# Kernel optimization log

Hardware: AMD Instinct MI355X
Metric: run time of the kernel (lower is better)

Reference implementation:

```python
import jax, jax.numpy as jnp
import numpy as np


def setup_inputs() -> dict:
    key = jax.random.key(0)
    ks = jax.random.split(key, 20)
    B, T, N, Cin = 1, 12, 30000, 16
    H, Hc = 64, 128
    O, KW = 12, 128
    E2 = 480000  # half of edges; symmetrized below -> E = 960000
    s = 0.05
    node_features = jax.random.normal(ks[0], (B, T, N, Cin), jnp.float32)
    src = jax.random.randint(ks[1], (T, E2), 0, N)
    dst = jax.random.randint(ks[2], (T, E2), 0, N)
    edge_index = jnp.concatenate(
        [jnp.stack([src, dst], axis=1), jnp.stack([dst, src], axis=1)], axis=-1)  # [T,2,E]
    return dict(
        node_features=node_features,
        edge_index=edge_index,
        gru_Wih0=jax.random.normal(ks[3], (2, 3 * H, Cin), jnp.float32) * s,
        gru_Whh0=jax.random.normal(ks[4], (2, 3 * H, H), jnp.float32) * s,
        gru_bih0=jax.random.normal(ks[5], (2, 3 * H), jnp.float32) * s,
        gru_bhh0=jax.random.normal(ks[6], (2, 3 * H), jnp.float32) * s,
        gru_Wih1=jax.random.normal(ks[7], (2, 3 * H, 2 * H), jnp.float32) * s,
        gru_Whh1=jax.random.normal(ks[8], (2, 3 * H, H), jnp.float32) * s,
        gru_bih1=jax.random.normal(ks[9], (2, 3 * H), jnp.float32) * s,
        gru_bhh1=jax.random.normal(ks[10], (2, 3 * H), jnp.float32) * s,
        ln_scale=jnp.ones((H,), jnp.float32),
        ln_bias=jnp.zeros((H,), jnp.float32),
        cheb_W=jax.random.normal(ks[11], (3, H, Hc), jnp.float32) * s,
        cheb_b=jnp.zeros((Hc,), jnp.float32),
        conv_W=jax.random.normal(ks[12], (O, T, 1, KW), jnp.float32) * s,
        conv_b=jnp.zeros((O,), jnp.float32),
    )


def reference(node_features, edge_index, gru_Wih0, gru_Whh0, gru_bih0, gru_bhh0,
              gru_Wih1, gru_Whh1, gru_bih1, gru_bhh1, ln_scale, ln_bias,
              cheb_W, cheb_b, conv_W, conv_b):
    B, T, N, Cin = node_features.shape
    H = gru_Whh0.shape[-1]
    M = B * N
    x = node_features.transpose(0, 2, 1, 3).reshape(M, T, Cin)

    def bigru(x, Wih, Whh, bih, bhh):
        # PyTorch bidirectional GRU layer (eval mode -> no dropout)
        outs = []
        for d, rev in ((0, False), (1, True)):
            gi = jnp.einsum('mtd,gd->tmg', x, Wih[d]) + bih[d]  # [T, M, 3H]
            def step(h, g, d=d):
                gh = h @ Whh[d].T + bhh[d]
                ir, iz, inn = jnp.split(g, 3, axis=-1)
                hr, hz, hn = jnp.split(gh, 3, axis=-1)
                r = jax.nn.sigmoid(ir + hr)
                z = jax.nn.sigmoid(iz + hz)
                n = jnp.tanh(inn + r * hn)
                h = (1.0 - z) * n + z * h
                return h, h
            h0 = jnp.zeros((x.shape[0], Whh.shape[-1]), x.dtype)
            _, ys = jax.lax.scan(step, h0, gi, reverse=rev)
            outs.append(jnp.swapaxes(ys, 0, 1))
        return jnp.concatenate(outs, axis=-1)  # [M, T, 2H]

    x = bigru(x, gru_Wih0, gru_Whh0, gru_bih0, gru_bhh0)
    x = bigru(x, gru_Wih1, gru_Whh1, gru_bih1, gru_bhh1)
    # reshape(M,T,2,H), LayerNorm(H), take direction 1 == slice then LayerNorm
    xb = x[:, :, H:]
    mu = jnp.mean(xb, axis=-1, keepdims=True)
    var = jnp.mean((xb - mu) ** 2, axis=-1, keepdims=True)
    xb = (xb - mu) * jax.lax.rsqrt(var + 1e-5) * ln_scale + ln_bias
    xs_t = jnp.moveaxis(xb.reshape(B, N, T, H), 2, 0).reshape(T, M, H)  # per-timestep [M,H]

    E = edge_index.shape[-1]
    N_ITER = 75  # power-iteration steps for lambda_max (scipy eigs equivalent)

    def cheb_step(_, inp):
        x_t, edges = inp  # x_t [M,H], edges [2,E]
        row, col = edges[0], edges[1]
        deg = jax.ops.segment_sum(jnp.ones((E,), x_t.dtype), row, num_segments=M)
        def Lmv(v):  # unnormalized Laplacian (D - A) matvec
            return deg * v - jax.ops.segment_sum(v[col], row, num_segments=M)
        v0 = jnp.full((M,), 1.0 / np.sqrt(M), x_t.dtype)
        def pit(i, v):
            w = Lmv(v)
            return w / (jnp.linalg.norm(w) + 1e-12)
        v = jax.lax.fori_loop(0, N_ITER, pit, v0)
        lam = jnp.vdot(v, Lmv(v))  # lambda_max of D - A (LaplacianLambdaMax default)
        # ChebConv sym-normalized, rescaled Laplacian: L_hat = (2/lam)*(I - D^-1/2 A D^-1/2) - I
        dinv = jnp.where(deg > 0, 1.0 / jnp.sqrt(jnp.maximum(deg, 1.0)), 0.0)
        we = (-2.0 / lam) * dinv[row] * dinv[col]  # off-diagonal weights
        diag = 2.0 / lam - 1.0                      # diagonal (all nodes)
        def Lhat(xm):
            return diag * xm + jax.ops.segment_sum(we[:, None] * xm[col], row, num_segments=M)
        Tx0 = x_t
        Tx1 = Lhat(Tx0)
        Tx2 = 2.0 * Lhat(Tx1) - Tx0
        out = Tx0 @ cheb_W[0] + Tx1 @ cheb_W[1] + Tx2 @ cheb_W[2] + cheb_b
        return 0, out

    _, emb = jax.lax.scan(cheb_step, 0, (xs_t, edge_index))  # [T, M, Hc]
    Hc = cheb_W.shape[-1]
    emb = jnp.moveaxis(emb.reshape(T, B, N, Hc), 0, 1)  # [B, T, N, Hc]
    # Conv2d(T -> O, kernel (1,KW)) followed by [:,:,:,-1]: only last window matters
    KW = conv_W.shape[-1]
    out = jnp.einsum('btnk,otk->bno', emb[..., Hc - KW:], conv_W[:, :, 0, :]) + conv_b
    return jax.nn.sigmoid(out)  # [B, N, num_for_predict]
```

## Files before the change

### kernel.cpp

```cpp
#include <hip/hip_runtime.h>
#include <hip/hip_bf16.h>

#define DEV __device__ __forceinline__

constexpr int Mn  = 30000;
constexpr int Tt  = 12;
constexpr int CIN = 16;
constexpr int Hh  = 64;
constexpr int Gg  = 192;
constexpr int C2  = 128;
constexpr int Ee  = 960000;
constexpr int HC  = 128;
constexpr int Oo  = 12;
constexpr int KW  = 128;
constexpr int SEGS= 938;
constexpr int NB  = 235;
constexpr int EPB = 8192;
constexpr int BPT = 118;
constexpr int CHK = 21;
constexpr int RC  = 1440;
constexpr int NRND= 76;
constexpr int NF4A= 21*256;
constexpr int NF4B= 20*104 + 44;

DEV float bf2f(__hip_bfloat16 v){ return __bfloat162float(v); }
DEV __hip_bfloat16 f2bf(float v){ return __float2bfloat16(v); }
DEV float sigm(float x){ return __builtin_amdgcn_rcpf(1.f + __expf(-x)); }
DEV float tanh_f(float x){ return 1.f - 2.f*__builtin_amdgcn_rcpf(__expf(2.f*x) + 1.f); }

DEV float aload_f(const float* p){ return __hip_atomic_load(p, __ATOMIC_RELAXED, __HIP_MEMORY_SCOPE_AGENT); }
DEV void  astore_f(float* p, float v){ __hip_atomic_store(p, v, __ATOMIC_RELAXED, __HIP_MEMORY_SCOPE_AGENT); }
DEV int   aload_i(const int* p){ return __hip_atomic_load(p, __ATOMIC_RELAXED, __HIP_MEMORY_SCOPE_AGENT); }
DEV void  astore_i(int* p, int v){ __hip_atomic_store(p, v, __ATOMIC_RELAXED, __HIP_MEMORY_SCOPE_AGENT); }
DEV unsigned long long aload_u64(const unsigned long long* p){ return __hip_atomic_load(p, __ATOMIC_RELAXED, __HIP_MEMORY_SCOPE_AGENT); }
DEV void astore_u64(unsigned long long* p, unsigned long long v){ __hip_atomic_store(p, v, __ATOMIC_RELAXED, __HIP_MEMORY_SCOPE_AGENT); }

typedef short bfrag8 __attribute__((ext_vector_type(8)));
typedef float ffrag4 __attribute__((ext_vector_type(4)));

DEV int off_h(int row, int col){
  return row*64 + ((((col >> 3) ^ (row & 7)) << 3) | (col & 7));
}

DEV short bfbits(float v){ __hip_bfloat16 b = f2bf(v); return *reinterpret_cast<short*>(&b); }

__global__ void k_init(int* bcnt, int* bfill, int* flagA, unsigned long long* pbB){
  int i = blockIdx.x*256 + threadIdx.x;
  if (i < Tt*CHK*16){ flagA[i] = 0; pbB[i] = 0ull; }
  if (i < Tt*NB){ bcnt[i] = 0; bfill[i] = 0; }
}

__global__ __launch_bounds__(256) void k_bcnt(const int* __restrict__ ei, int* __restrict__ bcnt){
  __shared__ int h[NB];
  const int b = blockIdx.x;
  const int w = (b & 7)*177 + (b >> 3);
  const int t = w / BPT, ch = w - t*BPT;
  const int e0 = ch*EPB;
  const int tid = threadIdx.x;
  for (int i = tid; i < NB; i += 256) h[i] = 0;
  __syncthreads();
  #pragma unroll
  for (int i = 0; i < 32; ++i){
    int e = e0 + i*256 + tid;
    if (e < Ee){
      int r = ei[(size_t)(t*2)*Ee + e];
      atomicAdd(&h[r >> 7], 1);
    }
  }
  __syncthreads();
  for (int i = tid; i < NB; i += 256){
    int c = h[i];
    if (c > 0) atomicAdd(&bcnt[t*NB + i], c);
  }
}

__global__ __launch_bounds__(256) void k_bscan(const int* __restrict__ bcnt, int* __restrict__ rpb){
  int t = blockIdx.x, tid = threadIdx.x;
  __shared__ int ps[256];
  int v = (tid < NB) ? bcnt[t*NB + tid] : 0;
  ps[tid] = v;
  __syncthreads();
  for (int o = 1; o < 256; o <<= 1){
    int x = (tid >= o) ? ps[tid-o] : 0;
    __syncthreads();
    ps[tid] += x;
    __syncthreads();
  }
  if (tid < NB) rpb[t*(NB+1) + tid] = ps[tid] - v;
  if (tid == 255) rpb[t*(NB+1) + NB] = ps[NB-1];
}

__global__ __launch_bounds__(256) void k_part2(const int* __restrict__ ei, const int* __restrict__ rpb,
    int* __restrict__ bfill, unsigned* __restrict__ pair){
  __shared__ int hcnt[NB];
  __shared__ int hbase[NB];
  const int b = blockIdx.x;
  const int w = (b & 7)*177 + (b >> 3);
  const int t = w / BPT, ch = w - t*BPT;
  const int e0 = ch*EPB;
  const int tid = threadIdx.x;
  for (int i = tid; i < NB; i += 256) hcnt[i] = 0;
  __syncthreads();
  unsigned key[32];
  #pragma unroll
  for (int i = 0; i < 32; ++i){
    int e = e0 + i*256 + tid;
    unsigned k = 0xFFFFFFFFu;
    if (e < Ee){
      int r = ei[(size_t)(t*2)*Ee + e];
      int c = ei[(size_t)(t*2+1)*Ee + e];
      k = ((unsigned)r << 16) | (unsigned)c;
      atomicAdd(&hcnt[r >> 7], 1);
    }
    key[i] = k;
  }
  __syncthreads();
  for (int i = tid; i < NB; i += 256){
    int cnt = hcnt[i];
    int base = (cnt > 0) ? atomicAdd(&bfill[t*NB + i], cnt) : 0;
    hbase[i] = rpb[t*(NB+1) + i] + base;
  }
  __syncthreads();
  for (int i = tid; i < NB; i += 256) hcnt[i] = 0;
  __syncthreads();
  #pragma unroll
  for (int i = 0; i < 32; ++i){
    unsigned k = key[i];
    if (k != 0xFFFFFFFFu){
      int r = (int)(k >> 16);
      int bk = r >> 7;
      int pos = atomicAdd(&hcnt[bk], 1);
      pair[(size_t)t*Ee + hbase[bk] + pos] = ((unsigned)(r & 127) << 16) | (k & 0xFFFFu);
    }
  }
}

__global__ __launch_bounds__(256) void k_csr2(const int* __restrict__ rpb, const unsigned* __restrict__ pair,
    unsigned short* __restrict__ col16, int* __restrict__ rp, int* __restrict__ deg){
  __shared__ unsigned short cols_s[9216];
  __shared__ int lcnt[128], lfill[128];
  __shared__ int ps[256];
  const int blk = blockIdx.x;
  const int t = blk / NB, bk = blk - t*NB;
  const int r0 = bk << 7;
  const int nr = (r0 + 128 <= Mn) ? 128 : (Mn - r0);
  const int base = rpb[t*(NB+1) + bk];
  const int cnt  = rpb[t*(NB+1) + bk + 1] - base;
  const int tid = threadIdx.x;
  if (tid < 128) lcnt[tid] = 0;
  __syncthreads();
  for (int i = tid; i < cnt; i += 256){
    unsigned v = pair[(size_t)t*Ee + base + i];
    atomicAdd(&lcnt[v >> 16], 1);
  }
  __syncthreads();
  int v2 = (tid < 128) ? lcnt[tid] : 0;
  ps[tid] = v2;
  __syncthreads();
  for (int o = 1; o < 128; o <<= 1){
    int x = (tid >= o) ? ps[tid-o] : 0;
    __syncthreads();
    ps[tid] += x;
    __syncthreads();
  }
  if (tid < 128){
    int excl = ps[tid] - v2;
    lfill[tid] = excl;
    if (tid < nr){
      rp[t*(Mn+1) + r0 + tid] = base + excl;
      deg[t*Mn + r0 + tid] = v2;
    }
  }
  if (bk == NB-1 && tid == 0) rp[t*(Mn+1) + Mn] = base + cnt;
  __syncthreads();
  for (int i = tid; i < cnt; i += 256){
    unsigned v = pair[(size_t)t*Ee + base + i];
    int pos = atomicAdd(&lfill[v >> 16], 1);
    cols_s[pos] = (unsigned short)(v & 0xFFFFu);
  }
  __syncthreads();
  for (int i = tid; i < cnt; i += 256)
    col16[(size_t)t*Ee + base + i] = cols_s[i];
}

__global__ void k_dinv(const int* __restrict__ deg, float* __restrict__ dinv){
  int i = blockIdx.x*256 + threadIdx.x;
  if (i < Tt*Mn){ int d = deg[i]; dinv[i] = (d > 0) ? rsqrtf((float)d) : 0.f; }
}

__global__ __launch_bounds__(256) void k_gru0(
    const float* __restrict__ nf, const float* __restrict__ Wih, const float* __restrict__ Whh,
    const float* __restrict__ bih, const float* __restrict__ bhh, __hip_bfloat16* __restrict__ y0)
{
  __shared__ __hip_bfloat16 xp[Tt*32*32];
  __shared__ __hip_bfloat16 h_hi[32*64];
  __shared__ __hip_bfloat16 h_lo[32*64];
  const int tid = threadIdx.x;
  const int m0  = blockIdx.x*32;
  const int lane = tid & 63, wv = tid >> 6;
  const int lr = lane & 15, lq = lane >> 4;
  for (int idx = tid; idx < Tt*32*CIN; idx += 256){
    int t = idx >> 9; int row = (idx >> 4) & 31; int k = idx & 15;
    int m = m0 + row;
    float v = (m < Mn) ? nf[((size_t)t*Mn + m)*CIN + k] : 0.f;
    __hip_bfloat16 hi = f2bf(v);
    xp[(t*32 + row)*32 + k]      = hi;
    xp[(t*32 + row)*32 + 16 + k] = f2bf(v - bf2f(hi));
  }
  for (int d = 0; d < 2; ++d){
    bfrag8 Bh[3][2], Bx[3];
    float b_r, b_z, b_in, b_hn;
    {
      const float* Wh = Whh + (size_t)d*Gg*Hh;
      const float* Wx = Wih + (size_t)d*Gg*CIN;
      #pragma unroll
      for (int c = 0; c < 3; ++c){
        int g = (wv + 4*c)*16 + lr;
        #pragma unroll
        for (int ks = 0; ks < 2; ++ks){
          bfrag8 f;
          #pragma unroll
          for (int r = 0; r < 8; ++r) f[r] = bfbits(Wh[(size_t)g*Hh + ks*32 + lq*8 + r]);
          Bh[c][ks] = f;
        }
        bfrag8 fx;
        #pragma unroll
        for (int r = 0; r < 8; ++r) fx[r] = bfbits(Wx[(size_t)g*CIN + ((lq*8 + r) & 15)]);
        Bx[c] = fx;
      }
      int j = wv*16 + lr;
      b_r  = bih[d*Gg + j]        + bhh[d*Gg + j];
      b_z  = bih[d*Gg + Hh + j]   + bhh[d*Gg + Hh + j];
      b_in = bih[d*Gg + 2*Hh + j];
      b_hn = bhh[d*Gg + 2*Hh + j];
    }
    float hreg[8];
    #pragma unroll
    for (int q = 0; q < 8; ++q) hreg[q] = 0.f;
    for (int i = tid; i < 32*64; i += 256){ h_hi[i] = f2bf(0.f); h_lo[i] = f2bf(0.f); }
    __syncthreads();
    for (int step = 0; step < Tt; ++step){
      int t = d ? (Tt-1-step) : step;
      bfrag8 xa[2], hhf[2][2], hlf[2][2];
      #pragma unroll
      for (int rt = 0; rt < 2; ++rt){
        int row = rt*16 + lr;
        xa[rt] = *(const bfrag8*)&xp[(t*32 + row)*32 + lq*8];
        #pragma unroll
        for (int ks = 0; ks < 2; ++ks){
          int e = off_h(row, ks*32 + lq*8);
          hhf[rt][ks] = *(const bfrag8*)&h_hi[e];
          hlf[rt][ks] = *(const bfrag8*)&h_lo[e];
        }
      }
      ffrag4 Cr[2], Cz[2], Cai[2], Cah[2];
      #pragma unroll
      for (int rt = 0; rt < 2; ++rt){
        ffrag4 z4 = (ffrag4){0.f,0.f,0.f,0.f};
        Cr[rt]  = __builtin_amdgcn_mfma_f32_16x16x32_bf16(xa[rt], Bx[0], z4, 0,0,0);
        Cz[rt]  = __builtin_amdgcn_mfma_f32_16x16x32_bf16(xa[rt], Bx[1], z4, 0,0,0);
        Cai[rt] = __builtin_amdgcn_mfma_f32_16x16x32_bf16(xa[rt], Bx[2], z4, 0,0,0);
        Cah[rt] = z4;
        #pragma unroll
        for (int ks = 0; ks < 2; ++ks){
          Cr[rt]  = __builtin_amdgcn_mfma_f32_16x16x32_bf16(hhf[rt][ks], Bh[0][ks], Cr[rt], 0,0,0);
          Cr[rt]  = __builtin_amdgcn_mfma_f32_16x16x32_bf16(hlf[rt][ks], Bh[0][ks], Cr[rt], 0,0,0);
          Cz[rt]  = __builtin_amdgcn_mfma_f32_16x16x32_bf16(hhf[rt][ks], Bh[1][ks], Cz[rt], 0,0,0);
          Cz[rt]  = __builtin_amdgcn_mfma_f32_16x16x32_bf16(hlf[rt][ks], Bh[1][ks], Cz[rt], 0,0,0);
          Cah[rt] = __builtin_amdgcn_mfma_f32_16x16x32_bf16(hhf[rt][ks], Bh[2][ks], Cah[rt], 0,0,0);
          Cah[rt] = __builtin_amdgcn_mfma_f32_16x16x32_bf16(hlf[rt][ks], Bh[2][ks], Cah[rt], 0,0,0);
        }
      }
      __syncthreads();
      #pragma unroll
      for (int rt = 0; rt < 2; ++rt){
        #pragma unroll
        for (int q = 0; q < 4; ++q){
          float r = sigm(Cr[rt][q] + b_r);
          float z = sigm(Cz[rt][q] + b_z);
          float n = tanh_f((Cai[rt][q] + b_in) + r*(Cah[rt][q] + b_hn));
          float h = (1.f - z)*n + z*hreg[rt*4+q];
          hreg[rt*4+q] = h;
          __hip_bfloat16 hi = f2bf(h);
          int e = off_h(rt*16 + lq*4 + q, wv*16 + lr);
          h_hi[e] = hi;
          h_lo[e] = f2bf(h - bf2f(hi));
        }
      }
      __syncthreads();
      {
        int row = tid >> 3, cg = tid & 7;
        int m = m0 + row;
        if (m < Mn){
          float4 v = *(const float4*)&h_hi[off_h(row, cg*8)];
          *(float4*)&y0[((size_t)t*Mn + m)*C2 + d*Hh + cg*8] = v;
        }
      }
    }
    __syncthreads();
  }
}

__global__ void k_wcvt(const float* __restrict__ W, __hip_bfloat16* __restrict__ Wbf){
  int i = blockIdx.x*256 + threadIdx.x;
  if (i < Gg*C2) Wbf[i] = f2bf(W[i]);
}

__global__ __launch_bounds__(256) void k_gi1m(const __hip_bfloat16* __restrict__ y0,
    const __hip_bfloat16* __restrict__ Wbf, const float* __restrict__ bih, __hip_bfloat16* __restrict__ gi)
{
  const int wid  = (blockIdx.x*256 + threadIdx.x) >> 6;
  const int lane = threadIdx.x & 63;
  if (wid >= Tt*SEGS) return;
  const int t = wid / SEGS, seg = wid - t*SEGS;
  const int m0 = seg*32;
  const int lr = lane & 15, lq = lane >> 4;
  const __hip_bfloat16* yb = y0 + (size_t)t*Mn*C2;

  ffrag4 acc[2][12];
  #pragma unroll
  for (int i = 0; i < 2; ++i){
    #pragma unroll
    for (int n = 0; n < 12; ++n) acc[i][n] = (ffrag4){0.f,0.f,0.f,0.f};
  }
  #pragma unroll
  for (int ks = 0; ks < 4; ++ks){
    const int ko = ks*32 + lq*8;
    bfrag8 a0 = *(const bfrag8*)(yb + (size_t)(m0 + lr     )*C2 + ko);
    bfrag8 a1 = *(const bfrag8*)(yb + (size_t)(m0 + 16 + lr)*C2 + ko);
    #pragma unroll
    for (int nt = 0; nt < 12; ++nt){
      bfrag8 b = *(const bfrag8*)(Wbf + (size_t)(nt*16 + lr)*C2 + ko);
      acc[0][nt] = __builtin_amdgcn_mfma_f32_16x16x32_bf16(a0, b, acc[0][nt], 0, 0, 0);
      acc[1][nt] = __builtin_amdgcn_mfma_f32_16x16x32_bf16(a1, b, acc[1][nt], 0, 0, 0);
    }
  }
  ushort4* go = (ushort4*)gi;
  #pragma unroll
  for (int i = 0; i < 2; ++i){
    #pragma unroll
    for (int nt = 0; nt < 12; ++nt){
      float bb = bih[nt*16 + lr];
      ushort4 pk;
      pk.x = (unsigned short)bfbits(acc[i][nt][0] + bb);
      pk.y = (unsigned short)bfbits(acc[i][nt][1] + bb);
      pk.z = (unsigned short)bfbits(acc[i][nt][2] + bb);
      pk.w = (unsigned short)bfbits(acc[i][nt][3] + bb);
      go[((((size_t)t*SEGS + seg)*2 + i)*12 + nt)*64 + lane] = pk;
    }
  }
}

__global__ __launch_bounds__(256) void k_gru1r(const __hip_bfloat16* __restrict__ gi,
    const float* __restrict__ Whh, const float* __restrict__ bhh,
    const float* __restrict__ lns, const float* __restrict__ lnb,
    __hip_bfloat16* __restrict__ xbt)
{
  __shared__ __hip_bfloat16 h_hi[32*64];
  __shared__ __hip_bfloat16 h_lo[32*64];
  __shared__ float h_f32[32*72];
  __shared__ float sc[Hh], bs[Hh];
  const int tid = threadIdx.x;
  const int seg = blockIdx.x;
  const int m0  = seg*32;
  const int lane = tid & 63, wv = tid >> 6;
  const int lr = lane & 15, lq = lane >> 4;
  bfrag8 Bh[3][2];
  float b_r, b_z, b_hn;
  #pragma unroll
  for (int c = 0; c < 3; ++c){
    int g = (wv + 4*c)*16 + lr;
    #pragma unroll
    for (int ks = 0; ks < 2; ++ks){
      bfrag8 f;
      #pragma unroll
      for (int r = 0; r < 8; ++r) f[r] = bfbits(Whh[(size_t)g*Hh + ks*32 + lq*8 + r]);
      Bh[c][ks] = f;
    }
  }
  {
    int j = wv*16 + lr;
    b_r  = bhh[j];
    b_z  = bhh[Hh + j];
    b_hn = bhh[2*Hh + j];
  }
  if (tid < Hh){ sc[tid] = lns[tid]; bs[tid] = lnb[tid]; }
  float hreg[8];
  #pragma unroll
  for (int q = 0; q < 8; ++q) hreg[q] = 0.f;
  for (int i = tid; i < 32*64; i += 256){ h_hi[i] = f2bf(0.f); h_lo[i] = f2bf(0.f); }
  __syncthreads();
  const ushort4* gbase = (const ushort4*)gi;
  for (int step = 0; step < Tt; ++step){
    int t = Tt-1-step;
    ffrag4 Cr[2], Cz[2], Cai[2], Cah[2];
    #pragma unroll
    for (int rt = 0; rt < 2; ++rt){
      size_t base = (((size_t)t*SEGS + seg)*2 + rt)*12;
      ushort4 gr4 = gbase[(base + wv     )*64 + lane];
      ushort4 gz4 = gbase[(base + wv + 4 )*64 + lane];
      ushort4 gn4 = gbase[(base + wv + 8 )*64 + lane];
      __hip_bfloat16 b;
      ffrag4 cr, cz, cn;
      b = *(__hip_bfloat16*)&gr4.x; cr[0] = bf2f(b);
      b = *(__hip_bfloat16*)&gr4.y; cr[1] = bf2f(b);
      b = *(__hip_bfloat16*)&gr4.z; cr[2] = bf2f(b);
      b = *(__hip_bfloat16*)&gr4.w; cr[3] = bf2f(b);
      b = *(__hip_bfloat16*)&gz4.x; cz[0] = bf2f(b);
      b = *(__hip_bfloat16*)&gz4.y; cz[1] = bf2f(b);
      b = *(__hip_bfloat16*)&gz4.z; cz[2] = bf2f(b);
      b = *(__hip_bfloat16*)&gz4.w; cz[3] = bf2f(b);
      b = *(__hip_bfloat16*)&gn4.x; cn[0] = bf2f(b);
      b = *(__hip_bfloat16*)&gn4.y; cn[1] = bf2f(b);
      b = *(__hip_bfloat16*)&gn4.z; cn[2] = bf2f(b);
      b = *(__hip_bfloat16*)&gn4.w; cn[3] = bf2f(b);
      Cr[rt] = cr; Cz[rt] = cz; Cai[rt] = cn;
      Cah[rt] = (ffrag4){0.f,0.f,0.f,0.f};
    }
    bfrag8 hhf[2][2], hlf[2][2];
    #pragma unroll
    for (int rt = 0; rt < 2; ++rt){
      int row = rt*16 + lr;
      #pragma unroll
      for (int ks = 0; ks < 2; ++ks){
        int e = off_h(row, ks*32 + lq*8);
        hhf[rt][ks] = *(const bfrag8*)&h_hi[e];
        hlf[rt][ks] = *(const bfrag8*)&h_lo[e];
      }
    }
    #pragma unroll
    for (int rt = 0; rt < 2; ++rt){
      #pragma unroll
      for (int ks = 0; ks < 2; ++ks){
        Cr[rt]  = __builtin_amdgcn_mfma_f32_16x16x32_bf16(hhf[rt][ks], Bh[0][ks], Cr[rt], 0,0,0);
        Cr[rt]  = __builtin_amdgcn_mfma_f32_16x16x32_bf16(hlf[rt][ks], Bh[0][ks], Cr[rt], 0,0,0);
        Cz[rt]  = __builtin_amdgcn_mfma_f32_16x16x32_bf16(hhf[rt][ks], Bh[1][ks], Cz[rt], 0,0,0);
        Cz[rt]  = __builtin_amdgcn_mfma_f32_16x16x32_bf16(hlf[rt][ks], Bh[1][ks], Cz[rt], 0,0,0);
        Cah[rt] = __builtin_amdgcn_mfma_f32_16x16x32_bf16(hhf[rt][ks], Bh[2][ks], Cah[rt], 0,0,0);
        Cah[rt] = __builtin_amdgcn_mfma_f32_16x16x32_bf16(hlf[rt][ks], Bh[2][ks], Cah[rt], 0,0,0);
      }
    }
    __syncthreads();
    #pragma unroll
    for (int rt = 0; rt < 2; ++rt){
      #pragma unroll
      for (int q = 0; q < 4; ++q){
        float r = sigm(Cr[rt][q] + b_r);
        float z = sigm(Cz[rt][q] + b_z);
        float n = tanh_f(Cai[rt][q] + r*(Cah[rt][q] + b_hn));
        float h = (1.f - z)*n + z*hreg[rt*4+q];
        hreg[rt*4+q] = h;
        __hip_bfloat16 hi = f2bf(h);
        int row = rt*16 + lq*4 + q;
        int e = off_h(row, wv*16 + lr);
        h_hi[e] = hi;
        h_lo[e] = f2bf(h - bf2f(hi));
        h_f32[row*72 + wv*16 + lr] = h;
      }
    }
    __syncthreads();
    {
      int row = tid >> 3, l = tid & 7;
      float4 v0 = *(const float4*)&h_f32[row*72 + l*8];
      float4 v1 = *(const float4*)&h_f32[row*72 + l*8 + 4];
      float vals[8] = {v0.x, v0.y, v0.z, v0.w, v1.x, v1.y, v1.z, v1.w};
      float s1 = 0.f, s2 = 0.f;
      #pragma unroll
      for (int q = 0; q < 8; ++q){ s1 += vals[q]; s2 += vals[q]*vals[q]; }
      #pragma unroll
      for (int off = 1; off <= 4; off <<= 1){ s1 += __shfl_xor(s1, off); s2 += __shfl_xor(s2, off); }
      float mu  = s1 * (1.f/64.f);
      float var = s2 * (1.f/64.f) - mu*mu;
      float rs  = rsqrtf(var + 1e-5f);
      int m = m0 + row;
      if (m < Mn){
        __hip_bfloat16 ob[8];
        #pragma unroll
        for (int q = 0; q < 8; ++q){ int j = l*8 + q; ob[q] = f2bf((vals[q]-mu)*rs*sc[j] + bs[j]); }
        *(float4*)&xbt[((size_t)t*Mn + m)*Hh + l*8] = *(float4*)ob;
      }
    }
    __syncthreads();
  }
}

__global__ __launch_bounds__(1024) void k_pitall(const int* __restrict__ rp,
    const unsigned short* __restrict__ col, float* __restrict__ urb,
    int* __restrict__ flagA, unsigned long long* __restrict__ pbB,
    float* __restrict__ lamc)
{
  __shared__ alignas(16) float u_s[Mn];
  __shared__ float redw[16];
  __shared__ float s_nrm;
  __shared__ int s_goA, s_goB;
  const int b = blockIdx.x;
  const int t = b / CHK, ch = b - t*CHK;
  const int r0 = ch*RC;
  const int r1 = (r0 + RC < Mn) ? r0 + RC : Mn;
  const int tid = threadIdx.x;
  const int lane = tid & 63;
  const int wv   = tid >> 6;
  const unsigned short* cp = col + (size_t)t*Ee;
  const int fS = t*CHK*16;
  const int pB = t*CHK*16;
  const int m0r = r0 + tid;
  const int m1r = m0r + 1024;
  int rb0 = 0, re0 = 0, rb1 = 0, re1 = 0;
  {
    const int* rpt = rp + t*(Mn+1);
    if (m0r < r1){ rb0 = rpt[m0r]; re0 = rpt[m0r+1]; }
    if (m1r < r1){ rb1 = rpt[m1r]; re1 = rpt[m1r+1]; }
  }
  if (tid == 0){ s_nrm = 1.0f; s_goA = 0; s_goB = 0; }
  __syncthreads();
  for (int r = 1; r <= NRND; ++r){
    const int fin = (r == NRND);
    if (r == 1){
      for (int i = tid; i < Mn; i += 1024) u_s[i] = 0.005773502691896258f;
    } else {
      const int rr = r - 1;
      const float4* u4 = (const float4*)(urb + (size_t)rr*(Tt*Mn) + (size_t)t*Mn);
      float4* s4 = (float4*)u_s;
      if (wv == 0){
        const bool mine = lane < CHK;
        for (;;){ int v = mine ? aload_i(&flagA[fS + lane*16]) : 0x7FFFFFFF;
                  if (__all(v >= rr)) break; __builtin_amdgcn_s_sleep(4); }
        if (lane == 0) __hip_atomic_store(&s_goA, rr, __ATOMIC_RELAXED, __HIP_MEMORY_SCOPE_WORKGROUP);
      } else {
        while (__hip_atomic_load(&s_goA, __ATOMIC_RELAXED, __HIP_MEMORY_SCOPE_WORKGROUP) < rr)
          __builtin_amdgcn_s_sleep(2);
      }
      asm volatile("" ::: "memory");
      for (int i = tid; i < NF4A; i += 1024){
        int idx = (i >> 8)*360 + (i & 255);
        s4[idx] = u4[idx];
      }
      unsigned long long pv = 0;
      if (wv == 0){
        const bool mine = lane < CHK;
        for (;;){ pv = mine ? aload_u64(&pbB[(size_t)(pB + lane*16) + (rr & 1)*8])
                            : ((unsigned long long)rr << 32);
                  if (__all((int)(pv >> 32) == rr)) break; __builtin_amdgcn_s_sleep(4); }
        if (lane == 0) __hip_atomic_store(&s_goB, rr, __ATOMIC_RELAXED, __HIP_MEMORY_SCOPE_WORKGROUP);
      } else {
        while (__hip_atomic_load(&s_goB, __ATOMIC_RELAXED, __HIP_MEMORY_SCOPE_WORKGROUP) < rr)
          __builtin_amdgcn_s_sleep(2);
      }
      asm volatile("" ::: "memory");
      for (int i = tid; i < NF4B; i += 1024){
        int ck = i/104, off = i - ck*104;
        int idx = ck*360 + 256 + off;
        s4[idx] = u4[idx];
      }
      if (wv == 0){
        float p = (lane < CHK) ? __uint_as_float((unsigned)pv) : 0.f;
        #pragma unroll
        for (int o2 = 1; o2 < 32; o2 <<= 1) p += __shfl_xor(p, o2);
        if (tid == 0) s_nrm = p;
      }
    }
    __syncthreads();
    const float inv_s = fin ? 1.f : 1.f/(sqrtf(s_nrm) + 1e-12f);
    float* u_ot = urb + (size_t)r*(Tt*Mn);
    float local = 0.f;
    if (m0r < r1){
      float s = 0.f;
      int i = rb0;
      for (; i < re0 && (i & 3); ++i) s += u_s[cp[i]];
      for (; i + 4 <= re0; i += 4){
        ushort4 c4 = *(const ushort4*)(cp + i);
        s += (u_s[c4.x] + u_s[c4.y]) + (u_s[c4.z] + u_s[c4.w]);
      }
      for (; i < re0; ++i) s += u_s[cp[i]];
      float uv = u_s[m0r];
      float wv2 = (float)(re0 - rb0)*uv - s;
      if (!fin){ float o = inv_s*wv2; astore_f(&u_ot[t*Mn + m0r], o); local += o*o; }
      else local += uv*wv2;
    }
    asm volatile("s_waitcnt vmcnt(0)" ::: "memory");
    __syncthreads();
    if (tid == 0) astore_i(&flagA[fS + ch*16], r);
    if (m1r < r1){
      float s = 0.f;
      int i = rb1;
      for (; i < re1 && (i & 3); ++i) s += u_s[cp[i]];
      for (; i + 4 <= re1; i += 4){
        ushort4 c4 = *(const ushort4*)(cp + i);
        s += (u_s[c4.x] + u_s[c4.y]) + (u_s[c4.z] + u_s[c4.w]);
      }
      for (; i < re1; ++i) s += u_s[cp[i]];
      float uv = u_s[m1r];
      float wv2 = (float)(re1 - rb1)*uv - s;
      if (!fin){ float o = inv_s*wv2; astore_f(&u_ot[t*Mn + m1r], o); local += o*o; }
      else local += uv*wv2;
    }
    #pragma unroll
    for (int o2 = 1; o2 < 64; o2 <<= 1) local += __shfl_xor(local, o2);
    if ((tid & 63) == 0) redw[tid >> 6] = local;
    asm volatile("s_waitcnt vmcnt(0)" ::: "memory");
    __syncthreads();
    if (tid < 64){
      float tot = (tid < 16) ? redw[tid] : 0.f;
      #pragma unroll
      for (int o2 = 1; o2 < 16; o2 <<= 1) tot += __shfl_xor(tot, o2);
      if (tid == 0){
        unsigned long long out = ((unsigned long long)r << 32)
                               | (unsigned long long)__float_as_uint(tot);
        astore_u64(&pbB[(size_t)(pB + ch*16) + (r & 1)*8], out);
      }
    }
  }
  if (ch == 0 && tid < 64){
    const bool mine = lane < CHK;
    unsigned long long pv = 0;
    for (;;){ pv = mine ? aload_u64(&pbB[(size_t)(pB + lane*16) + (NRND & 1)*8])
                        : ((unsigned long long)NRND << 32);
              if (__all((int)(pv >> 32) == NRND)) break; __builtin_amdgcn_s_sleep(4); }
    float p = mine ? __uint_as_float((unsigned)pv) : 0.f;
    #pragma unroll
    for (int o2 = 1; o2 < 32; o2 <<= 1) p += __shfl_xor(p, o2);
    if (tid == 0){
      float nn = sqrtf(s_nrm) + 1e-12f;
      float lam = p / (nn*nn);
      lamc[2*t+0] = -2.f/lam;
      lamc[2*t+1] =  2.f/lam - 1.f;
    }
  }
}

__global__ __launch_bounds__(256) void k_cheb(const __hip_bfloat16* __restrict__ xin,
    const __hip_bfloat16* __restrict__ xb0, __hip_bfloat16* __restrict__ outp,
    const int* __restrict__ rp, const unsigned short* __restrict__ col,
    const float* __restrict__ dinv, const float* __restrict__ lamc, float s1, float s2)
{
  const int blk = blockIdx.x;
  const int w = (blk & 7)*11250 + (blk >> 3);
  const int gw = w*4 + (threadIdx.x >> 6);
  const int lane = threadIdx.x & 63;
  int t = gw / Mn, m = gw - t*Mn;
  float coef = lamc[2*t], diag = lamc[2*t+1];
  const __hip_bfloat16* xt = xin + (size_t)t*Mn*Hh;
  const float* dv = dinv + t*Mn;
  float acc = diag * bf2f(xt[(size_t)m*Hh + lane]);
  float cdm = coef * dv[m];
  int bgn = rp[t*(Mn+1)+m], end = rp[t*(Mn+1)+m+1];
  const unsigned short* cp = col + (size_t)t*Ee;
  int i = bgn;
  for (; i < end && (i & 3); ++i){ int c = cp[i]; acc += (cdm*dv[c])*bf2f(xt[(size_t)c*Hh + lane]); }
  for (; i + 4 <= end; i += 4){
    ushort4 c4 = *(const ushort4*)(cp + i);
    float w0 = cdm*dv[c4.x], w1 = cdm*dv[c4.y], w2 = cdm*dv[c4.z], w3 = cdm*dv[c4.w];
    acc += w0*bf2f(xt[(size_t)c4.x*Hh + lane]);
    acc += w1*bf2f(xt[(size_t)c4.y*Hh + lane]);
    acc += w2*bf2f(xt[(size_t)c4.z*Hh + lane]);
    acc += w3*bf2f(xt[(size_t)c4.w*Hh + lane]);
  }
  for (; i < end; ++i){ int c = cp[i]; acc += (cdm*dv[c])*bf2f(xt[(size_t)c*Hh + lane]); }
  float o = s1*acc;
  if (s2 != 0.f) o += s2*bf2f(xb0[(size_t)gw*Hh + lane]);
  outp[(size_t)gw*Hh + lane] = f2bf(o);
}

__global__ void k_ww(const float* __restrict__ chebW, const float* __restrict__ chebb,
    const float* __restrict__ convW, const float* __restrict__ convb, float* __restrict__ WW, float* __restrict__ c0)
{
  int idx = blockIdx.x*256 + threadIdx.x;
  if (idx < 3*Tt*Hh*Oo){
    int oc = idx % Oo; int j = (idx/Oo) % Hh; int t = (idx/(Oo*Hh)) % Tt; int i = idx/(Oo*Hh*Tt);
    const float* cw = chebW + ((size_t)i*Hh + j)*HC + (HC-KW);
    const float* vw = convW + ((size_t)oc*Tt + t)*KW;
    float s = 0.f;
    for (int k = 0; k < KW; ++k) s += cw[k]*vw[k];
    WW[idx] = s;
  }
  if (blockIdx.x == 0 && threadIdx.x < Oo){
    int oc = threadIdx.x;
    float s = convb[oc];
    for (int t = 0; t < Tt; ++t){
      const float* vw = convW + ((size_t)oc*Tt + t)*KW;
      for (int k = 0; k < KW; ++k) s += chebb[(HC-KW)+k]*vw[k];
    }
    c0[oc] = s;
  }
}

__global__ __launch_bounds__(256) void k_final(const __hip_bfloat16* __restrict__ tx0,
    const __hip_bfloat16* __restrict__ tx1, const __hip_bfloat16* __restrict__ tx2,
    const float* __restrict__ WW, const float* __restrict__ c0, float* __restrict__ outp)
{
  __shared__ float xs[64][65];
  __shared__ float ww[64][12];
  const int tid = threadIdx.x;
  const int n0 = blockIdx.x*64;
  const int n = tid & 63, ob = (tid >> 6)*3;
  float acc[3] = {0.f, 0.f, 0.f};
  for (int it = 0; it < 3*Tt; ++it){
    int ii = it / Tt, t = it % Tt;
    const __hip_bfloat16* tx = (ii == 0) ? tx0 : (ii == 1) ? tx1 : tx2;
    __syncthreads();
    for (int idx = tid; idx < 64*64; idx += 256){
      int mm = idx >> 6, j = idx & 63;
      int m = n0 + mm;
      xs[mm][j] = (m < Mn) ? bf2f(tx[((size_t)t*Mn + m)*Hh + j]) : 0.f;
    }
    for (int idx = tid; idx < 64*Oo; idx += 256)
      ((float*)ww)[idx] = WW[((size_t)(ii*Tt + t)*Hh)*Oo + idx];
    __syncthreads();
    #pragma unroll 8
    for (int j = 0; j < 64; ++j){
      float x = xs[n][j];
      acc[0] += x*ww[j][ob+0];
      acc[1] += x*ww[j][ob+1];
      acc[2] += x*ww[j][ob+2];
    }
  }
  int m = n0 + n;
  if (m < Mn){
    #pragma unroll
    for (int q = 0; q < 3; ++q) outp[(size_t)m*Oo + ob + q] = sigm(acc[q] + c0[ob+q]);
  }
}

extern "C" void kernel_launch(void* const* d_in, const int* in_sizes, int n_in,
                              void* d_out, int out_size, void* d_ws, size_t ws_size,
                              hipStream_t stream)
{
  const float* nf    = (const float*)d_in[0];
  const int*   ei    = (const int*)d_in[1];
  const float* Wih0  = (const float*)d_in[2];
  const float* Whh0  = (const float*)d_in[3];
  const float* bih0  = (const float*)d_in[4];
  const float* bhh0  = (const float*)d_in[5];
  const float* Wih1  = (const float*)d_in[6];
  const float* Whh1  = (const float*)d_in[7];
  const float* bih1  = (const float*)d_in[8];
  const float* bhh1  = (const float*)d_in[9];
  const float* lns   = (const float*)d_in[10];
  const float* lnb   = (const float*)d_in[11];
  const float* chebW = (const float*)d_in[12];
  const float* chebb = (const float*)d_in[13];
  const float* convW = (const float*)d_in[14];
  const float* convb = (const float*)d_in[15];
  float* outp = (float*)d_out;

  char* base = (char*)d_ws;
  size_t off = 0;
  auto alloc = [&](size_t bytes)->char*{ char* p = base + off; off += (bytes + 255) & ~(size_t)255; return p; };

  __hip_bfloat16* y0  = (__hip_bfloat16*)alloc((size_t)Tt*Mn*C2*2);
  __hip_bfloat16* tx1 = y0;
  __hip_bfloat16* tx2 = y0 + (size_t)Tt*Mn*Hh;
  __hip_bfloat16* gi  = (__hip_bfloat16*)alloc((size_t)Tt*SEGS*32*Gg*2);
  unsigned* pair = (unsigned*)gi;
  float* urb = (float*)gi;
  __hip_bfloat16* xbt = (__hip_bfloat16*)alloc((size_t)Tt*Mn*Hh*2);
  unsigned short* col16 = (unsigned short*)alloc((size_t)Tt*Ee*2);
  int*   deg  = (int*)alloc((size_t)Tt*Mn*4);
  int*   rp   = (int*)alloc((size_t)Tt*(Mn+1)*4);
  int*   bcnt = (int*)alloc((size_t)Tt*NB*4);
  int*   bfill= (int*)alloc((size_t)Tt*NB*4);
  int*   rpb  = (int*)alloc((size_t)Tt*(NB+1)*4);
  float* dinv = (float*)alloc((size_t)Tt*Mn*4);
  float* lamc = (float*)alloc((size_t)2*Tt*4);
  float* WW   = (float*)alloc((size_t)3*Tt*Hh*Oo*4);
  float* c0   = (float*)alloc((size_t)Oo*4);
  __hip_bfloat16* Wbf = (__hip_bfloat16*)alloc((size_t)Gg*C2*2);
  int*   flagA = (int*)alloc((size_t)Tt*CHK*16*4);
  unsigned long long* pbB = (unsigned long long*)alloc((size_t)Tt*CHK*16*8);
  (void)ws_size; (void)in_sizes; (void)n_in; (void)out_size;

  k_init<<<16, 256, 0, stream>>>(bcnt, bfill, flagA, pbB);
  k_bcnt<<<Tt*BPT, 256, 0, stream>>>(ei, bcnt);
  k_bscan<<<Tt, 256, 0, stream>>>(bcnt, rpb);
  k_part2<<<Tt*BPT, 256, 0, stream>>>(ei, rpb, bfill, pair);
  k_csr2<<<Tt*NB, 256, 0, stream>>>(rpb, pair, col16, rp, deg);
  k_dinv<<<(Tt*Mn + 255)/256, 256, 0, stream>>>(deg, dinv);

  k_wcvt<<<(Gg*C2 + 255)/256, 256, 0, stream>>>(Wih1 + (size_t)Gg*C2, Wbf);
  k_gru0<<<SEGS, 256, 0, stream>>>(nf, Wih0, Whh0, bih0, bhh0, y0);
  {
    int waves = Tt*SEGS;
    k_gi1m<<<(waves + 3)/4, 256, 0, stream>>>(y0, Wbf, bih1 + Gg, gi);
  }
  k_gru1r<<<SEGS, 256, 0, stream>>>(gi, Whh1 + (size_t)Gg*Hh, bhh1 + Gg, lns, lnb, xbt);

  k_pitall<<<Tt*CHK, 1024, 0, stream>>>(rp, col16, urb, flagA, pbB, lamc);

  k_cheb<<<(Tt*Mn)/4, 256, 0, stream>>>(xbt, xbt, tx1, rp, col16, dinv, lamc, 1.f, 0.f);
  k_cheb<<<(Tt*Mn)/4, 256, 0, stream>>>(tx1, xbt, tx2, rp, col16, dinv, lamc, 2.f, -1.f);

  k_ww<<<(3*Tt*Hh*Oo + 255)/256, 256, 0, stream>>>(chebW, chebb, convW, convb, WW, c0);
  k_final<<<(Mn + 63)/64, 256, 0, stream>>>(xbt, tx1, tx2, WW, c0, outp);
}
```

Measured before the change: 2.557 ms.

## Fuse layer-1 input projection into reverse GRU kernel and dinv into CSR build

The separate k_gi1m GEMM that wrote the bf16 gate-input tensor to global memory is removed. k_gru1r now holds the input-weight fragments in registers and computes the input projection with MFMA inside each timestep, folding bih into the biases. The dinv computation also moves into k_csr2, which drops the deg buffer and a launch. This avoids a large write and read of the gi intermediate, at the cost of more registers and MFMA work inside the sequential recurrence kernel, which runs only SEGS blocks.

```diff
diff --git a/kernel.cpp b/kernel.cpp
--- a/kernel.cpp
+++ b/kernel.cpp
@@ -136,7 +136,7 @@
 }
 
 __global__ __launch_bounds__(256) void k_csr2(const int* __restrict__ rpb, const unsigned* __restrict__ pair,
-    unsigned short* __restrict__ col16, int* __restrict__ rp, int* __restrict__ deg){
+    unsigned short* __restrict__ col16, int* __restrict__ rp, float* __restrict__ dinv){
   __shared__ unsigned short cols_s[9216];
   __shared__ int lcnt[128], lfill[128];
   __shared__ int ps[256];
@@ -168,7 +168,7 @@
     lfill[tid] = excl;
     if (tid < nr){
       rp[t*(Mn+1) + r0 + tid] = base + excl;
-      deg[t*Mn + r0 + tid] = v2;
+      dinv[t*Mn + r0 + tid] = (v2 > 0) ? rsqrtf((float)v2) : 0.f;
     }
   }
   if (bk == NB-1 && tid == 0) rp[t*(Mn+1) + Mn] = base + cnt;
@@ -181,11 +181,6 @@
   __syncthreads();
   for (int i = tid; i < cnt; i += 256)
     col16[(size_t)t*Ee + base + i] = cols_s[i];
-}
-
-__global__ void k_dinv(const int* __restrict__ deg, float* __restrict__ dinv){
-  int i = blockIdx.x*256 + threadIdx.x;
-  if (i < Tt*Mn){ int d = deg[i]; dinv[i] = (d > 0) ? rsqrtf((float)d) : 0.f; }
 }
 
 __global__ __launch_bounds__(256) void k_gru0(
@@ -306,53 +301,9 @@
   if (i < Gg*C2) Wbf[i] = f2bf(W[i]);
 }
 
-__global__ __launch_bounds__(256) void k_gi1m(const __hip_bfloat16* __restrict__ y0,
-    const __hip_bfloat16* __restrict__ Wbf, const float* __restrict__ bih, __hip_bfloat16* __restrict__ gi)
-{
-  const int wid  = (blockIdx.x*256 + threadIdx.x) >> 6;
-  const int lane = threadIdx.x & 63;
-  if (wid >= Tt*SEGS) return;
-  const int t = wid / SEGS, seg = wid - t*SEGS;
-  const int m0 = seg*32;
-  const int lr = lane & 15, lq = lane >> 4;
-  const __hip_bfloat16* yb = y0 + (size_t)t*Mn*C2;
-
-  ffrag4 acc[2][12];
-  #pragma unroll
-  for (int i = 0; i < 2; ++i){
-    #pragma unroll
-    for (int n = 0; n < 12; ++n) acc[i][n] = (ffrag4){0.f,0.f,0.f,0.f};
-  }
-  #pragma unroll
-  for (int ks = 0; ks < 4; ++ks){
-    const int ko = ks*32 + lq*8;
-    bfrag8 a0 = *(const bfrag8*)(yb + (size_t)(m0 + lr     )*C2 + ko);
-    bfrag8 a1 = *(const bfrag8*)(yb + (size_t)(m0 + 16 + lr)*C2 + ko);
-    #pragma unroll
-    for (int nt = 0; nt < 12; ++nt){
-      bfrag8 b = *(const bfrag8*)(Wbf + (size_t)(nt*16 + lr)*C2 + ko);
-      acc[0][nt] = __builtin_amdgcn_mfma_f32_16x16x32_bf16(a0, b, acc[0][nt], 0, 0, 0);
-      acc[1][nt] = __builtin_amdgcn_mfma_f32_16x16x32_bf16(a1, b, acc[1][nt], 0, 0, 0);
-    }
-  }
-  ushort4* go = (ushort4*)gi;
-  #pragma unroll
-  for (int i = 0; i < 2; ++i){
-    #pragma unroll
-    for (int nt = 0; nt < 12; ++nt){
-      float bb = bih[nt*16 + lr];
-      ushort4 pk;
-      pk.x = (unsigned short)bfbits(acc[i][nt][0] + bb);
-      pk.y = (unsigned short)bfbits(acc[i][nt][1] + bb);
-      pk.z = (unsigned short)bfbits(acc[i][nt][2] + bb);
-      pk.w = (unsigned short)bfbits(acc[i][nt][3] + bb);
-      go[((((size_t)t*SEGS + seg)*2 + i)*12 + nt)*64 + lane] = pk;
-    }
-  }
-}
-
-__global__ __launch_bounds__(256) void k_gru1r(const __hip_bfloat16* __restrict__ gi,
-    const float* __restrict__ Whh, const float* __restrict__ bhh,
+__global__ __launch_bounds__(256) void k_gru1r(const __hip_bfloat16* __restrict__ y0,
+    const __hip_bfloat16* __restrict__ Wbf, const float* __restrict__ Whh,
+    const float* __restrict__ bih, const float* __restrict__ bhh,
     const float* __restrict__ lns, const float* __restrict__ lnb,
     __hip_bfloat16* __restrict__ xbt)
 {
@@ -366,7 +317,6 @@
   const int lane = tid & 63, wv = tid >> 6;
   const int lr = lane & 15, lq = lane >> 4;
   bfrag8 Bh[3][2];
-  float b_r, b_z, b_hn;
   #pragma unroll
   for (int c = 0; c < 3; ++c){
     int g = (wv + 4*c)*16 + lr;
@@ -378,11 +328,21 @@
       Bh[c][ks] = f;
     }
   }
+  bfrag8 Bp[3][4];
+  #pragma unroll
+  for (int c = 0; c < 3; ++c){
+    int g = (wv + 4*c)*16 + lr;
+    #pragma unroll
+    for (int ks = 0; ks < 4; ++ks)
+      Bp[c][ks] = *(const bfrag8*)(Wbf + (size_t)g*C2 + ks*32 + lq*8);
+  }
+  float b_r, b_z, b_in, b_hn;
   {
     int j = wv*16 + lr;
-    b_r  = bhh[j];
-    b_z  = bhh[Hh + j];
-    b_hn = bhh[2*Hh + j];
+    b_r  = bih[j]      + bhh[j];
+    b_z  = bih[Hh+j]   + bhh[Hh+j];
+    b_in = bih[2*Hh+j];
+    b_hn = bhh[2*Hh+j];
   }
   if (tid < Hh){ sc[tid] = lns[tid]; bs[tid] = lnb[tid]; }
   float hreg[8];
@@ -390,32 +350,26 @@
   for (int q = 0; q < 8; ++q) hreg[q] = 0.f;
   for (int i = tid; i < 32*64; i += 256){ h_hi[i] = f2bf(0.f); h_lo[i] = f2bf(0.f); }
   __syncthreads();
-  const ushort4* gbase = (const ushort4*)gi;
   for (int step = 0; step < Tt; ++step){
     int t = Tt-1-step;
+    const __hip_bfloat16* yb = y0 + (size_t)t*Mn*C2;
     ffrag4 Cr[2], Cz[2], Cai[2], Cah[2];
     #pragma unroll
     for (int rt = 0; rt < 2; ++rt){
-      size_t base = (((size_t)t*SEGS + seg)*2 + rt)*12;
-      ushort4 gr4 = gbase[(base + wv     )*64 + lane];
-      ushort4 gz4 = gbase[(base + wv + 4 )*64 + lane];
-      ushort4 gn4 = gbase[(base + wv + 8 )*64 + lane];
-      __hip_bfloat16 b;
-      ffrag4 cr, cz, cn;
-      b = *(__hip_bfloat16*)&gr4.x; cr[0] = bf2f(b);
-      b = *(__hip_bfloat16*)&gr4.y; cr[1] = bf2f(b);
-      b = *(__hip_bfloat16*)&gr4.z; cr[2] = bf2f(b);
-      b = *(__hip_bfloat16*)&gr4.w; cr[3] = bf2f(b);
-      b = *(__hip_bfloat16*)&gz4.x; cz[0] = bf2f(b);
-      b = *(__hip_bfloat16*)&gz4.y; cz[1] = bf2f(b);
-      b = *(__hip_bfloat16*)&gz4.z; cz[2] = bf2f(b);
-      b = *(__hip_bfloat16*)&gz4.w; cz[3] = bf2f(b);
-      b = *(__hip_bfloat16*)&gn4.x; cn[0] = bf2f(b);
-      b = *(__hip_bfloat16*)&gn4.y; cn[1] = bf2f(b);
-      b = *(__hip_bfloat16*)&gn4.z; cn[2] = bf2f(b);
-      b = *(__hip_bfloat16*)&gn4.w; cn[3] = bf2f(b);
-      Cr[rt] = cr; Cz[rt] = cz; Cai[rt] = cn;
-      Cah[rt] = (ffrag4){0.f,0.f,0.f,0.f};
+      ffrag4 z4 = (ffrag4){0.f,0.f,0.f,0.f};
+      Cr[rt] = z4; Cz[rt] = z4; Cai[rt] = z4; Cah[rt] = z4;
+    }
+    #pragma unroll
+    for (int ks = 0; ks < 4; ++ks){
+      const int ko = ks*32 + lq*8;
+      bfrag8 a0 = *(const bfrag8*)(yb + (size_t)(m0 + lr     )*C2 + ko);
+      bfrag8 a1 = *(const bfrag8*)(yb + (size_t)(m0 + 16 + lr)*C2 + ko);
+      Cr[0]  = __builtin_amdgcn_mfma_f32_16x16x32_bf16(a0, Bp[0][ks], Cr[0], 0,0,0);
+      Cr[1]  = __builtin_amdgcn_mfma_f32_16x16x32_bf16(a1, Bp[0][ks], Cr[1], 0,0,0);
+      Cz[0]  = __builtin_amdgcn_mfma_f32_16x16x32_bf16(a0, Bp[1][ks], Cz[0], 0,0,0);
+      Cz[1]  = __builtin_amdgcn_mfma_f32_16x16x32_bf16(a1, Bp[1][ks], Cz[1], 0,0,0);
+      Cai[0] = __builtin_amdgcn_mfma_f32_16x16x32_bf16(a0, Bp[2][ks], Cai[0], 0,0,0);
+      Cai[1] = __builtin_amdgcn_mfma_f32_16x16x32_bf16(a1, Bp[2][ks], Cai[1], 0,0,0);
     }
     bfrag8 hhf[2][2], hlf[2][2];
     #pragma unroll
@@ -447,7 +401,7 @@
       for (int q = 0; q < 4; ++q){
         float r = sigm(Cr[rt][q] + b_r);
         float z = sigm(Cz[rt][q] + b_z);
-        float n = tanh_f(Cai[rt][q] + r*(Cah[rt][q] + b_hn));
+        float n = tanh_f((Cai[rt][q] + b_in) + r*(Cah[rt][q] + b_hn));
         float h = (1.f - z)*n + z*hreg[rt*4+q];
         hreg[rt*4+q] = h;
         __hip_bfloat16 hi = f2bf(h);
@@ -750,12 +704,11 @@
   __hip_bfloat16* y0  = (__hip_bfloat16*)alloc((size_t)Tt*Mn*C2*2);
   __hip_bfloat16* tx1 = y0;
   __hip_bfloat16* tx2 = y0 + (size_t)Tt*Mn*Hh;
-  __hip_bfloat16* gi  = (__hip_bfloat16*)alloc((size_t)Tt*SEGS*32*Gg*2);
-  unsigned* pair = (unsigned*)gi;
-  float* urb = (float*)gi;
+  char* arena = alloc((size_t)(NRND+1)*Tt*Mn*4);
+  unsigned* pair = (unsigned*)arena;
+  float*    urb  = (float*)arena;
   __hip_bfloat16* xbt = (__hip_bfloat16*)alloc((size_t)Tt*Mn*Hh*2);
   unsigned short* col16 = (unsigned short*)alloc((size_t)Tt*Ee*2);
-  int*   deg  = (int*)alloc((size_t)Tt*Mn*4);
   int*   rp   = (int*)alloc((size_t)Tt*(Mn+1)*4);
   int*   bcnt = (int*)alloc((size_t)Tt*NB*4);
   int*   bfill= (int*)alloc((size_t)Tt*NB*4);
@@ -773,16 +726,12 @@
   k_bcnt<<<Tt*BPT, 256, 0, stream>>>(ei, bcnt);
   k_bscan<<<Tt, 256, 0, stream>>>(bcnt, rpb);
   k_part2<<<Tt*BPT, 256, 0, stream>>>(ei, rpb, bfill, pair);
-  k_csr2<<<Tt*NB, 256, 0, stream>>>(rpb, pair, col16, rp, deg);
-  k_dinv<<<(Tt*Mn + 255)/256, 256, 0, stream>>>(deg, dinv);
+  k_csr2<<<Tt*NB, 256, 0, stream>>>(rpb, pair, col16, rp, dinv);
 
   k_wcvt<<<(Gg*C2 + 255)/256, 256, 0, stream>>>(Wih1 + (size_t)Gg*C2, Wbf);
   k_gru0<<<SEGS, 256, 0, stream>>>(nf, Wih0, Whh0, bih0, bhh0, y0);
-  {
-    int waves = Tt*SEGS;
-    k_gi1m<<<(waves + 3)/4, 256, 0, stream>>>(y0, Wbf, bih1 + Gg, gi);
-  }
-  k_gru1r<<<SEGS, 256, 0, stream>>>(gi, Whh1 + (size_t)Gg*Hh, bhh1 + Gg, lns, lnb, xbt);
+  k_gru1r<<<SEGS, 256, 0, stream>>>(y0, Wbf, Whh1 + (size_t)Gg*Hh,
+                                    bih1 + Gg, bhh1 + Gg, lns, lnb, xbt);
 
   k_pitall<<<Tt*CHK, 1024, 0, stream>>>(rp, col16, urb, flagA, pbB, lamc);
 
```

Result: faster. 2.483 ms (-2.9%).
